# Optimization experiments

Measured on AMD Instinct MI355X. Metric: run time of the kernel, lower is better.

## Reference

```python
import jax, jax.numpy as jnp
import numpy as np

N = 150000   # nodes
E = 600000   # edges
F_IN = 32    # node features
H = 128      # hidden_channels == MLP_neurons
G = 2048     # graphs in batch


def setup_inputs() -> dict:
    key = jax.random.key(0)
    ks = iter(jax.random.split(key, 40))
    inp = {}
    inp['x'] = jax.random.normal(next(ks), (N, F_IN), dtype=jnp.float32)
    inp['edge_index'] = jax.random.randint(next(ks), (2, E), 0, N)
    inp['batch'] = jnp.sort(jax.random.randint(next(ks), (N,), 0, G))
    # GINConv MLPs: Linear(in,H) ReLU Linear(H,H) ReLU Linear(H,H)
    for i, f_in in enumerate([F_IN, H, H]):
        s1 = 1.0 / np.sqrt(f_in)
        s2 = 1.0 / np.sqrt(H)
        inp[f'c{i}_w1'] = jax.random.uniform(next(ks), (f_in, H), minval=-s1, maxval=s1)
        inp[f'c{i}_b1'] = jnp.zeros((H,), jnp.float32)
        inp[f'c{i}_w2'] = jax.random.uniform(next(ks), (H, H), minval=-s2, maxval=s2)
        inp[f'c{i}_b2'] = jnp.zeros((H,), jnp.float32)
        inp[f'c{i}_w3'] = jax.random.uniform(next(ks), (H, H), minval=-s2, maxval=s2)
        inp[f'c{i}_b3'] = jnp.zeros((H,), jnp.float32)
    s = 1.0 / np.sqrt(H)
    inp['fc0_w'] = jax.random.uniform(next(ks), (H, H), minval=-s, maxval=s)
    inp['fc0_b'] = jnp.zeros((H,), jnp.float32)
    inp['fc1_w'] = jax.random.uniform(next(ks), (H, H), minval=-s, maxval=s)
    inp['fc1_b'] = jnp.zeros((H,), jnp.float32)
    inp['out_w'] = jax.random.uniform(next(ks), (H, 2), minval=-s, maxval=s)
    inp['out_b'] = jnp.zeros((2,), jnp.float32)
    return inp


def _gin_layer(x, edge_index, w1, b1, w2, b2, w3, b3):
    # GINConv with eps=0: h = MLP(x + sum_{j in N(i)} x_j)
    agg = jax.ops.segment_sum(x[edge_index[0]], edge_index[1], num_segments=N)
    h = x + agg
    h = jax.nn.relu(h @ w1 + b1)
    h = jax.nn.relu(h @ w2 + b2)
    h = h @ w3 + b3
    return jax.nn.relu(h)  # outer .relu() in forward


def reference(x, edge_index, batch,
              c0_w1, c0_b1, c0_w2, c0_b2, c0_w3, c0_b3,
              c1_w1, c1_b1, c1_w2, c1_b2, c1_w3, c1_b3,
              c2_w1, c2_b1, c2_w2, c2_b2, c2_w3, c2_b3,
              fc0_w, fc0_b, fc1_w, fc1_b, out_w, out_b):
    h = _gin_layer(x, edge_index, c0_w1, c0_b1, c0_w2, c0_b2, c0_w3, c0_b3)
    h = _gin_layer(h, edge_index, c1_w1, c1_b1, c1_w2, c1_b2, c1_w3, c1_b3)
    h = _gin_layer(h, edge_index, c2_w1, c2_b1, c2_w2, c2_b2, c2_w3, c2_b3)
    # global_mean_pool over graph ids
    sums = jax.ops.segment_sum(h, batch, num_segments=G)            # [G,H]
    cnts = jax.ops.segment_sum(jnp.ones((N,), h.dtype), batch, num_segments=G)
    g = sums / jnp.maximum(cnts, 1.0)[:, None]
    # classifier head (dropout is identity at inference)
    g = jax.nn.relu(g @ fc0_w + fc0_b)
    g = jax.nn.relu(g @ fc1_w + fc1_b)
    return g @ out_w + out_b  # [G,2]
```

## Files before the change

### kernel.cpp

```cpp
#include <hip/hip_runtime.h>
#include <hip/hip_bf16.h>

#define NN 150000
#define EE 600000
#define F_IN 32
#define HD 128
#define GG 2048
#define CAP 28
#define NP 150016

typedef __attribute__((ext_vector_type(8))) short bf16x8;
typedef __attribute__((ext_vector_type(4))) float f32x4;

__device__ inline void split_bf16(float v, unsigned short& hi, unsigned short& lo) {
    __hip_bfloat16 h = __float2bfloat16(v);
    float hv = __bfloat162float(h);
    __hip_bfloat16 l = __float2bfloat16(v - hv);
    hi = *reinterpret_cast<unsigned short*>(&h);
    lo = *reinterpret_cast<unsigned short*>(&l);
}
__device__ inline unsigned short bf16_hi(float v) {
    __hip_bfloat16 h = __float2bfloat16(v);
    return *reinterpret_cast<unsigned short*>(&h);
}
__device__ inline unsigned short bf16_lo(float v) {
    __hip_bfloat16 h = __float2bfloat16(v);
    float hv = __bfloat162float(h);
    __hip_bfloat16 l = __float2bfloat16(v - hv);
    return *reinterpret_cast<unsigned short*>(&l);
}
__device__ inline float bf2f(unsigned short u) {
    union { unsigned int i; float f; } c;
    c.i = ((unsigned int)u) << 16;
    return c.f;
}

__global__ void init_zero(int* __restrict__ cnt_node, int* __restrict__ cntg,
                          float* __restrict__ pooled) {
    int i = blockIdx.x * blockDim.x + threadIdx.x;
    if (i < NN) cnt_node[i] = 0;
    if (i < GG) cntg[i] = 0;
    if (i < GG * HD) pooled[i] = 0.f;
}

__global__ void build_graph(const int* __restrict__ ei, const int* __restrict__ batch,
                            int* __restrict__ cnt_node, int* __restrict__ cntg,
                            int* __restrict__ bucket) {
    int e = blockIdx.x * blockDim.x + threadIdx.x;
    if (e < NN) atomicAdd(&cntg[batch[e]], 1);
    if (e >= EE) return;
    int src = ei[e];
    int dst = ei[EE + e];
    int slot = atomicAdd(&cnt_node[dst], 1);
    if (slot < CAP) bucket[dst * CAP + slot] = src;
}

struct PrepDesc { const float* src; unsigned short* dhi; unsigned short* dlo; int K; };
struct PrepArgs { PrepDesc d[9]; };

__global__ void prep_weights(PrepArgs pa) {
    PrepDesc de = pa.d[blockIdx.y];
    int total = de.K * HD;
    int KS = de.K >> 5;
    for (int idx = blockIdx.x * blockDim.x + threadIdx.x; idx < total;
         idx += gridDim.x * blockDim.x) {
        int k = idx / HD, h = idx - (idx / HD) * HD;
        unsigned short hi, lo;
        split_bf16(de.src[idx], hi, lo);
        int nt = h >> 4, m = h & 15;
        int ks = k >> 5, quad = (k >> 3) & 3, e = k & 7;
        int lane = quad * 16 + m;
        int pidx = ((nt * KS + ks) * 64 + lane) * 8 + e;
        de.dhi[pidx] = hi;
        de.dlo[pidx] = lo;
    }
}

template <int K_IN, bool BF16IN, bool POOL>
__launch_bounds__(256, 3)
__global__ void gin_layer(const void* __restrict__ hin_,
                          const int* __restrict__ cnt_node,
                          const int* __restrict__ bucket,
                          const unsigned short* __restrict__ w1h, const unsigned short* __restrict__ w1l,
                          const float* __restrict__ b1,
                          const unsigned short* __restrict__ w2h, const unsigned short* __restrict__ w2l,
                          const float* __restrict__ b2,
                          const unsigned short* __restrict__ w3h, const unsigned short* __restrict__ w3l,
                          const float* __restrict__ b3,
                          unsigned short* __restrict__ out,
                          const int* __restrict__ batch,
                          float* __restrict__ pooled) {
    constexpr int KS1 = K_IN / 32;
    constexpr int UN = BF16IN ? 4 : (KS1 == 1 ? 8 : 2);
    __shared__ unsigned short sh[4][32][HD + 8];

    const int wave = threadIdx.x >> 6;
    const int lane = threadIdx.x & 63;
    const int m = lane & 15;
    const int quad = lane >> 4;
    const int nodeBase = blockIdx.x * 128 + wave * 32;

    const float* hf = (const float*)hin_;
    const unsigned short* hb = (const unsigned short*)hin_;

    bf16x8 ah[2][KS1], al[2][KS1];
#pragma unroll
    for (int s = 0; s < 2; s++) {
        int node = nodeBase + s * 16 + m;
        node = node < NN ? node : NN - 1;
        float ag[KS1][8];
        if (BF16IN) {
            const unsigned short* rs = hb + (size_t)node * K_IN + quad * 8;
#pragma unroll
            for (int ks = 0; ks < KS1; ks++) {
                bf16x8 v = *(const bf16x8*)(rs + ks * 32);
#pragma unroll
                for (int e = 0; e < 8; e++) ag[ks][e] = bf2f((unsigned short)v[e]);
            }
        } else {
            const float* rs = hf + (size_t)node * K_IN + quad * 8;
#pragma unroll
            for (int ks = 0; ks < KS1; ks++) {
                float4 v0 = *(const float4*)(rs + ks * 32);
                float4 v1 = *(const float4*)(rs + ks * 32 + 4);
                ag[ks][0] = v0.x; ag[ks][1] = v0.y; ag[ks][2] = v0.z; ag[ks][3] = v0.w;
                ag[ks][4] = v1.x; ag[ks][5] = v1.y; ag[ks][6] = v1.z; ag[ks][7] = v1.w;
            }
        }
        int cnt = cnt_node[node];
        cnt = cnt < CAP ? cnt : CAP;
        const int* b = bucket + (size_t)node * CAP;
        int i = 0;
        if (BF16IN) {
            for (; i + UN <= cnt; i += UN) {
                bf16x8 v[UN][KS1];
#pragma unroll
                for (int j = 0; j < UN; j++) {
                    const unsigned short* r = hb + (size_t)b[i + j] * K_IN + quad * 8;
#pragma unroll
                    for (int ks = 0; ks < KS1; ks++)
                        v[j][ks] = *(const bf16x8*)(r + ks * 32);
                }
#pragma unroll
                for (int ks = 0; ks < KS1; ks++)
#pragma unroll
                    for (int e = 0; e < 8; e++) {
                        float t01 = bf2f((unsigned short)v[0][ks][e]) +
                                    bf2f((unsigned short)v[1][ks][e]);
                        float t23 = bf2f((unsigned short)v[2][ks][e]) +
                                    bf2f((unsigned short)v[3][ks][e]);
                        ag[ks][e] += t01 + t23;
                    }
            }
            for (; i < cnt; i++) {
                const unsigned short* r = hb + (size_t)b[i] * K_IN + quad * 8;
#pragma unroll
                for (int ks = 0; ks < KS1; ks++) {
                    bf16x8 v = *(const bf16x8*)(r + ks * 32);
#pragma unroll
                    for (int e = 0; e < 8; e++) ag[ks][e] += bf2f((unsigned short)v[e]);
                }
            }
        } else {
            for (; i + UN <= cnt; i += UN) {
                float4 v0[UN][KS1], v1[UN][KS1];
#pragma unroll
                for (int j = 0; j < UN; j++) {
                    const float* r = hf + (size_t)b[i + j] * K_IN + quad * 8;
#pragma unroll
                    for (int ks = 0; ks < KS1; ks++) {
                        v0[j][ks] = *(const float4*)(r + ks * 32);
                        v1[j][ks] = *(const float4*)(r + ks * 32 + 4);
                    }
                }
#pragma unroll
                for (int ks = 0; ks < KS1; ks++) {
#pragma unroll
                    for (int e = 0; e < 4; e++) {
                        float s01 = (&v0[0][ks].x)[e] + (&v0[1][ks].x)[e];
                        float s23 = (&v0[2][ks].x)[e] + (&v0[3][ks].x)[e];
                        if (UN == 8) {
                            s01 += (&v0[4][ks].x)[e] + (&v0[5][ks].x)[e];
                            s23 += (&v0[6][ks].x)[e] + (&v0[7][ks].x)[e];
                        }
                        ag[ks][e] += s01 + s23;
                    }
#pragma unroll
                    for (int e = 0; e < 4; e++) {
                        float s01 = (&v1[0][ks].x)[e] + (&v1[1][ks].x)[e];
                        float s23 = (&v1[2][ks].x)[e] + (&v1[3][ks].x)[e];
                        if (UN == 8) {
                            s01 += (&v1[4][ks].x)[e] + (&v1[5][ks].x)[e];
                            s23 += (&v1[6][ks].x)[e] + (&v1[7][ks].x)[e];
                        }
                        ag[ks][e + 4] += s01 + s23;
                    }
                }
            }
            for (; i < cnt; i++) {
                const float* r = hf + (size_t)b[i] * K_IN + quad * 8;
#pragma unroll
                for (int ks = 0; ks < KS1; ks++) {
                    float4 v0 = *(const float4*)(r + ks * 32);
                    float4 v1 = *(const float4*)(r + ks * 32 + 4);
                    ag[ks][0] += v0.x; ag[ks][1] += v0.y; ag[ks][2] += v0.z; ag[ks][3] += v0.w;
                    ag[ks][4] += v1.x; ag[ks][5] += v1.y; ag[ks][6] += v1.z; ag[ks][7] += v1.w;
                }
            }
        }
#pragma unroll
        for (int ks = 0; ks < KS1; ks++) {
            bf16x8 vh, vl;
#pragma unroll
            for (int e = 0; e < 8; e++) {
                unsigned short hi, lo;
                split_bf16(ag[ks][e], hi, lo);
                vh[e] = (short)hi;
                vl[e] = (short)lo;
            }
            ah[s][ks] = vh;
            al[s][ks] = vl;
        }
    }

    f32x4 acc[2][8];

#pragma unroll
    for (int nt = 0; nt < 8; nt++) {
        bf16x8 bh[KS1], bl[KS1];
#pragma unroll
        for (int ks = 0; ks < KS1; ks++) {
            bh[ks] = *(const bf16x8*)(w1h + ((nt * KS1 + ks) * 64 + lane) * 8);
            bl[ks] = *(const bf16x8*)(w1l + ((nt * KS1 + ks) * 64 + lane) * 8);
        }
        f32x4 c0 = {0.f, 0.f, 0.f, 0.f};
        f32x4 c1 = {0.f, 0.f, 0.f, 0.f};
#pragma unroll
        for (int ks = 0; ks < KS1; ks++) {
            c0 = __builtin_amdgcn_mfma_f32_16x16x32_bf16(ah[0][ks], bh[ks], c0, 0, 0, 0);
            c1 = __builtin_amdgcn_mfma_f32_16x16x32_bf16(ah[1][ks], bh[ks], c1, 0, 0, 0);
            c0 = __builtin_amdgcn_mfma_f32_16x16x32_bf16(al[0][ks], bh[ks], c0, 0, 0, 0);
            c1 = __builtin_amdgcn_mfma_f32_16x16x32_bf16(al[1][ks], bh[ks], c1, 0, 0, 0);
            c0 = __builtin_amdgcn_mfma_f32_16x16x32_bf16(ah[0][ks], bl[ks], c0, 0, 0, 0);
            c1 = __builtin_amdgcn_mfma_f32_16x16x32_bf16(ah[1][ks], bl[ks], c1, 0, 0, 0);
        }
        acc[0][nt] = c0;
        acc[1][nt] = c1;
    }

    bf16x8 a2h[2][4], a2l[2][4];
#pragma unroll
    for (int s = 0; s < 2; s++)
#pragma unroll
        for (int nt = 0; nt < 8; nt++) {
            float bj = b1[nt * 16 + m];
#pragma unroll
            for (int r = 0; r < 4; r++)
                sh[wave][s * 16 + quad * 4 + r][nt * 16 + m] =
                    bf16_hi(fmaxf(acc[s][nt][r] + bj, 0.f));
        }
#pragma unroll
    for (int s = 0; s < 2; s++)
#pragma unroll
        for (int ks = 0; ks < 4; ks++)
            a2h[s][ks] = *(const bf16x8*)&sh[wave][s * 16 + m][ks * 32 + quad * 8];
#pragma unroll
    for (int s = 0; s < 2; s++)
#pragma unroll
        for (int nt = 0; nt < 8; nt++) {
            float bj = b1[nt * 16 + m];
#pragma unroll
            for (int r = 0; r < 4; r++)
                sh[wave][s * 16 + quad * 4 + r][nt * 16 + m] =
                    bf16_lo(fmaxf(acc[s][nt][r] + bj, 0.f));
        }
#pragma unroll
    for (int s = 0; s < 2; s++)
#pragma unroll
        for (int ks = 0; ks < 4; ks++)
            a2l[s][ks] = *(const bf16x8*)&sh[wave][s * 16 + m][ks * 32 + quad * 8];

#pragma unroll
    for (int nt = 0; nt < 8; nt++) {
        bf16x8 bh[4], bl[4];
#pragma unroll
        for (int ks = 0; ks < 4; ks++) {
            bh[ks] = *(const bf16x8*)(w2h + ((nt * 4 + ks) * 64 + lane) * 8);
            bl[ks] = *(const bf16x8*)(w2l + ((nt * 4 + ks) * 64 + lane) * 8);
        }
        f32x4 c0 = {0.f, 0.f, 0.f, 0.f};
        f32x4 c1 = {0.f, 0.f, 0.f, 0.f};
#pragma unroll
        for (int ks = 0; ks < 4; ks++) {
            c0 = __builtin_amdgcn_mfma_f32_16x16x32_bf16(a2h[0][ks], bh[ks], c0, 0, 0, 0);
            c1 = __builtin_amdgcn_mfma_f32_16x16x32_bf16(a2h[1][ks], bh[ks], c1, 0, 0, 0);
            c0 = __builtin_amdgcn_mfma_f32_16x16x32_bf16(a2l[0][ks], bh[ks], c0, 0, 0, 0);
            c1 = __builtin_amdgcn_mfma_f32_16x16x32_bf16(a2l[1][ks], bh[ks], c1, 0, 0, 0);
            c0 = __builtin_amdgcn_mfma_f32_16x16x32_bf16(a2h[0][ks], bl[ks], c0, 0, 0, 0);
            c1 = __builtin_amdgcn_mfma_f32_16x16x32_bf16(a2h[1][ks], bl[ks], c1, 0, 0, 0);
        }
        acc[0][nt] = c0;
        acc[1][nt] = c1;
    }

#pragma unroll
    for (int s = 0; s < 2; s++)
#pragma unroll
        for (int nt = 0; nt < 8; nt++) {
            float bj = b2[nt * 16 + m];
#pragma unroll
            for (int r = 0; r < 4; r++)
                sh[wave][s * 16 + quad * 4 + r][nt * 16 + m] =
                    bf16_hi(fmaxf(acc[s][nt][r] + bj, 0.f));
        }
#pragma unroll
    for (int s = 0; s < 2; s++)
#pragma unroll
        for (int ks = 0; ks < 4; ks++)
            a2h[s][ks] = *(const bf16x8*)&sh[wave][s * 16 + m][ks * 32 + quad * 8];
#pragma unroll
    for (int s = 0; s < 2; s++)
#pragma unroll
        for (int nt = 0; nt < 8; nt++) {
            float bj = b2[nt * 16 + m];
#pragma unroll
            for (int r = 0; r < 4; r++)
                sh[wave][s * 16 + quad * 4 + r][nt * 16 + m] =
                    bf16_lo(fmaxf(acc[s][nt][r] + bj, 0.f));
        }
#pragma unroll
    for (int s = 0; s < 2; s++)
#pragma unroll
        for (int ks = 0; ks < 4; ks++)
            a2l[s][ks] = *(const bf16x8*)&sh[wave][s * 16 + m][ks * 32 + quad * 8];

#pragma unroll
    for (int nt = 0; nt < 8; nt++) {
        bf16x8 bh[4], bl[4];
#pragma unroll
        for (int ks = 0; ks < 4; ks++) {
            bh[ks] = *(const bf16x8*)(w3h + ((nt * 4 + ks) * 64 + lane) * 8);
            bl[ks] = *(const bf16x8*)(w3l + ((nt * 4 + ks) * 64 + lane) * 8);
        }
        f32x4 c0 = {0.f, 0.f, 0.f, 0.f};
        f32x4 c1 = {0.f, 0.f, 0.f, 0.f};
#pragma unroll
        for (int ks = 0; ks < 4; ks++) {
            c0 = __builtin_amdgcn_mfma_f32_16x16x32_bf16(a2h[0][ks], bh[ks], c0, 0, 0, 0);
            c1 = __builtin_amdgcn_mfma_f32_16x16x32_bf16(a2h[1][ks], bh[ks], c1, 0, 0, 0);
            c0 = __builtin_amdgcn_mfma_f32_16x16x32_bf16(a2l[0][ks], bh[ks], c0, 0, 0, 0);
            c1 = __builtin_amdgcn_mfma_f32_16x16x32_bf16(a2l[1][ks], bh[ks], c1, 0, 0, 0);
            c0 = __builtin_amdgcn_mfma_f32_16x16x32_bf16(a2h[0][ks], bl[ks], c0, 0, 0, 0);
            c1 = __builtin_amdgcn_mfma_f32_16x16x32_bf16(a2h[1][ks], bl[ks], c1, 0, 0, 0);
        }
        acc[0][nt] = c0;
        acc[1][nt] = c1;
    }

    if (POOL) {
        float* shf = (float*)&sh[wave][0][0];
#pragma unroll
        for (int h = 0; h < 2; h++) {
#pragma unroll
            for (int nt = 0; nt < 8; nt++) {
                float bj = b3[nt * 16 + m];
#pragma unroll
                for (int r = 0; r < 4; r++)
                    shf[(quad * 4 + r) * 132 + nt * 16 + m] =
                        fmaxf(acc[h][nt][r] + bj, 0.f);
            }
            int c0 = lane * 2;
            float run0 = 0.f, run1 = 0.f;
            int gp = -1;
            for (int rrow = 0; rrow < 16; rrow++) {
                int node = nodeBase + h * 16 + rrow;
                if (node >= NN) break;
                int g = batch[node];
                float2 xv = *(const float2*)&shf[rrow * 132 + c0];
                if (g != gp) {
                    if (gp >= 0) {
                        atomicAdd(&pooled[(size_t)gp * HD + c0 + 0], run0);
                        atomicAdd(&pooled[(size_t)gp * HD + c0 + 1], run1);
                    }
                    run0 = xv.x; run1 = xv.y; gp = g;
                } else {
                    run0 += xv.x; run1 += xv.y;
                }
            }
            if (gp >= 0) {
                atomicAdd(&pooled[(size_t)gp * HD + c0 + 0], run0);
                atomicAdd(&pooled[(size_t)gp * HD + c0 + 1], run1);
            }
        }
    } else {
#pragma unroll
        for (int s = 0; s < 2; s++)
#pragma unroll
            for (int nt = 0; nt < 8; nt++) {
                float bj = b3[nt * 16 + m];
#pragma unroll
                for (int r = 0; r < 4; r++)
                    sh[wave][s * 16 + quad * 4 + r][nt * 16 + m] =
                        bf16_hi(fmaxf(acc[s][nt][r] + bj, 0.f));
            }
#pragma unroll
        for (int io = 0; io < 8; io++) {
            int row32 = io * 4 + quad;
            int col = m * 8;
            int n2 = nodeBase + row32;
            bf16x8 v = *(const bf16x8*)&sh[wave][row32][col];
            if (n2 < NN) *(bf16x8*)&out[(size_t)n2 * HD + col] = v;
        }
    }
}

__launch_bounds__(128)
__global__ void head(const float* __restrict__ pooled, const int* __restrict__ cntg,
                     const float* __restrict__ fc0_w, const float* __restrict__ fc0_b,
                     const float* __restrict__ fc1_w, const float* __restrict__ fc1_b,
                     const float* __restrict__ out_w, const float* __restrict__ out_b,
                     float* __restrict__ out) {
    int g = blockIdx.x;
    int j = threadIdx.x;
    __shared__ float s0[HD];
    __shared__ float s1[HD];
    int c = cntg[g];
    float cf = (float)(c > 1 ? c : 1);
    s0[j] = pooled[(size_t)g * HD + j] / cf;
    __syncthreads();

    float acc = fc0_b[j];
    for (int k = 0; k < HD; k += 4) {
        float4 hv = *(const float4*)&s0[k];
        acc = fmaf(hv.x, fc0_w[(k + 0) * HD + j], acc);
        acc = fmaf(hv.y, fc0_w[(k + 1) * HD + j], acc);
        acc = fmaf(hv.z, fc0_w[(k + 2) * HD + j], acc);
        acc = fmaf(hv.w, fc0_w[(k + 3) * HD + j], acc);
    }
    s1[j] = fmaxf(acc, 0.0f);
    __syncthreads();

    acc = fc1_b[j];
    for (int k = 0; k < HD; k += 4) {
        float4 hv = *(const float4*)&s1[k];
        acc = fmaf(hv.x, fc1_w[(k + 0) * HD + j], acc);
        acc = fmaf(hv.y, fc1_w[(k + 1) * HD + j], acc);
        acc = fmaf(hv.z, fc1_w[(k + 2) * HD + j], acc);
        acc = fmaf(hv.w, fc1_w[(k + 3) * HD + j], acc);
    }
    float v = fmaxf(acc, 0.0f);

    float p0 = v * out_w[j * 2 + 0];
    float p1 = v * out_w[j * 2 + 1];
    __syncthreads();
    s0[j] = p0;
    s1[j] = p1;
    __syncthreads();
    for (int off = 64; off >= 1; off >>= 1) {
        if (j < off) {
            s0[j] += s0[j + off];
            s1[j] += s1[j + off];
        }
        __syncthreads();
    }
    if (j == 0) {
        out[(size_t)g * 2 + 0] = s0[0] + out_b[0];
        out[(size_t)g * 2 + 1] = s1[0] + out_b[1];
    }
}

extern "C" void kernel_launch(void* const* d_in, const int* in_sizes, int n_in,
                              void* d_out, int out_size, void* d_ws, size_t ws_size,
                              hipStream_t stream) {
    const float* x     = (const float*)d_in[0];
    const int*   ei    = (const int*)d_in[1];
    const int*   batch = (const int*)d_in[2];
    const float* cw[3][6];
    for (int i = 0; i < 3; i++)
        for (int k = 0; k < 6; k++) cw[i][k] = (const float*)d_in[3 + 6 * i + k];
    const float* fc0_w = (const float*)d_in[21];
    const float* fc0_b = (const float*)d_in[22];
    const float* fc1_w = (const float*)d_in[23];
    const float* fc1_b = (const float*)d_in[24];
    const float* out_w = (const float*)d_in[25];
    const float* out_b = (const float*)d_in[26];
    float* out = (float*)d_out;

    char* ws = (char*)d_ws;
    size_t off = 0;
    auto carve = [&](size_t bytes) {
        void* p = ws + off;
        off += (bytes + 255) & ~(size_t)255;
        return p;
    };
    int*   cnt_node = (int*)carve((size_t)NN * 4);
    int*   cntg     = (int*)carve((size_t)GG * 4);
    float* pooled   = (float*)carve((size_t)GG * HD * 4);
    int*   bucket   = (int*)carve((size_t)NN * CAP * 4);
    unsigned short* hA = (unsigned short*)carve((size_t)NP * HD * 2);
    unsigned short* hB = (unsigned short*)carve((size_t)NP * HD * 2);
    unsigned short* wHi[9];
    unsigned short* wLo[9];
    int wK[9] = {F_IN, HD, HD, HD, HD, HD, HD, HD, HD};
    for (int i = 0; i < 9; i++) {
        wHi[i] = (unsigned short*)carve((size_t)wK[i] * HD * 2);
        wLo[i] = (unsigned short*)carve((size_t)wK[i] * HD * 2);
    }
    (void)ws_size;

    init_zero<<<(GG * HD + 255) / 256, 256, 0, stream>>>(cnt_node, cntg, pooled);
    build_graph<<<(EE + 255) / 256, 256, 0, stream>>>(ei, batch, cnt_node, cntg, bucket);

    PrepArgs pa;
    for (int l = 0; l < 3; l++)
        for (int s = 0; s < 3; s++) {
            int i = l * 3 + s;
            pa.d[i].src = cw[l][2 * s];
            pa.d[i].dhi = wHi[i];
            pa.d[i].dlo = wLo[i];
            pa.d[i].K = wK[i];
        }
    prep_weights<<<dim3(16, 9), 256, 0, stream>>>(pa);

    const int blocks = NP / 128;

    gin_layer<F_IN, false, false><<<blocks, 256, 0, stream>>>(x, cnt_node, bucket,
        wHi[0], wLo[0], cw[0][1], wHi[1], wLo[1], cw[0][3], wHi[2], wLo[2], cw[0][5],
        hA, batch, pooled);
    gin_layer<HD, true, false><<<blocks, 256, 0, stream>>>(hA, cnt_node, bucket,
        wHi[3], wLo[3], cw[1][1], wHi[4], wLo[4], cw[1][3], wHi[5], wLo[5], cw[1][5],
        hB, batch, pooled);
    gin_layer<HD, true, true><<<blocks, 256, 0, stream>>>(hB, cnt_node, bucket,
        wHi[6], wLo[6], cw[2][1], wHi[7], wLo[7], cw[2][3], wHi[8], wLo[8], cw[2][5],
        nullptr, batch, pooled);

    head<<<GG, 128, 0, stream>>>(pooled, cntg, fc0_w, fc0_b, fc1_w, fc1_b, out_w, out_b, out);
}
```

Measured before the change: 547.2 us.

## Transpose neighbor bucket layout, replace graph-count atomics with binary search

```diff
diff --git a/kernel.cpp b/kernel.cpp
--- a/kernel.cpp
+++ b/kernel.cpp
@@ -35,24 +35,15 @@
     return c.f;
 }
 
-__global__ void init_zero(int* __restrict__ cnt_node, int* __restrict__ cntg,
-                          float* __restrict__ pooled) {
-    int i = blockIdx.x * blockDim.x + threadIdx.x;
-    if (i < NN) cnt_node[i] = 0;
-    if (i < GG) cntg[i] = 0;
-    if (i < GG * HD) pooled[i] = 0.f;
-}
-
-__global__ void build_graph(const int* __restrict__ ei, const int* __restrict__ batch,
-                            int* __restrict__ cnt_node, int* __restrict__ cntg,
+__global__ void build_graph(const int* __restrict__ ei,
+                            int* __restrict__ cnt_node,
                             int* __restrict__ bucket) {
     int e = blockIdx.x * blockDim.x + threadIdx.x;
-    if (e < NN) atomicAdd(&cntg[batch[e]], 1);
     if (e >= EE) return;
     int src = ei[e];
     int dst = ei[EE + e];
     int slot = atomicAdd(&cnt_node[dst], 1);
-    if (slot < CAP) bucket[dst * CAP + slot] = src;
+    if (slot < CAP) bucket[slot * NN + dst] = src;
 }
 
 struct PrepDesc { const float* src; unsigned short* dhi; unsigned short* dlo; int K; };
@@ -129,14 +120,14 @@
         }
         int cnt = cnt_node[node];
         cnt = cnt < CAP ? cnt : CAP;
-        const int* b = bucket + (size_t)node * CAP;
+        const int* b = bucket + node;
         int i = 0;
         if (BF16IN) {
             for (; i + UN <= cnt; i += UN) {
                 bf16x8 v[UN][KS1];
 #pragma unroll
                 for (int j = 0; j < UN; j++) {
-                    const unsigned short* r = hb + (size_t)b[i + j] * K_IN + quad * 8;
+                    const unsigned short* r = hb + (size_t)b[(i + j) * NN] * K_IN + quad * 8;
 #pragma unroll
                     for (int ks = 0; ks < KS1; ks++)
                         v[j][ks] = *(const bf16x8*)(r + ks * 32);
@@ -153,7 +144,7 @@
                     }
             }
             for (; i < cnt; i++) {
-                const unsigned short* r = hb + (size_t)b[i] * K_IN + quad * 8;
+                const unsigned short* r = hb + (size_t)b[i * NN] * K_IN + quad * 8;
 #pragma unroll
                 for (int ks = 0; ks < KS1; ks++) {
                     bf16x8 v = *(const bf16x8*)(r + ks * 32);
@@ -166,7 +157,7 @@
                 float4 v0[UN][KS1], v1[UN][KS1];
 #pragma unroll
                 for (int j = 0; j < UN; j++) {
-                    const float* r = hf + (size_t)b[i + j] * K_IN + quad * 8;
+                    const float* r = hf + (size_t)b[(i + j) * NN] * K_IN + quad * 8;
 #pragma unroll
                     for (int ks = 0; ks < KS1; ks++) {
                         v0[j][ks] = *(const float4*)(r + ks * 32);
@@ -198,7 +189,7 @@
                 }
             }
             for (; i < cnt; i++) {
-                const float* r = hf + (size_t)b[i] * K_IN + quad * 8;
+                const float* r = hf + (size_t)b[i * NN] * K_IN + quad * 8;
 #pragma unroll
                 for (int ks = 0; ks < KS1; ks++) {
                     float4 v0 = *(const float4*)(r + ks * 32);
@@ -414,8 +405,17 @@
     }
 }
 
+__device__ inline int lb_batch(const int* __restrict__ batch, int key) {
+    int lo = 0, hi = NN;
+    while (lo < hi) {
+        int mid = (lo + hi) >> 1;
+        if (batch[mid] < key) lo = mid + 1; else hi = mid;
+    }
+    return lo;
+}
+
 __launch_bounds__(128)
-__global__ void head(const float* __restrict__ pooled, const int* __restrict__ cntg,
+__global__ void head(const float* __restrict__ pooled, const int* __restrict__ batch,
                      const float* __restrict__ fc0_w, const float* __restrict__ fc0_b,
                      const float* __restrict__ fc1_w, const float* __restrict__ fc1_b,
                      const float* __restrict__ out_w, const float* __restrict__ out_b,
@@ -424,7 +424,7 @@
     int j = threadIdx.x;
     __shared__ float s0[HD];
     __shared__ float s1[HD];
-    int c = cntg[g];
+    int c = lb_batch(batch, g + 1) - lb_batch(batch, g);
     float cf = (float)(c > 1 ? c : 1);
     s0[j] = pooled[(size_t)g * HD + j] / cf;
     __syncthreads();
@@ -494,7 +494,6 @@
         return p;
     };
     int*   cnt_node = (int*)carve((size_t)NN * 4);
-    int*   cntg     = (int*)carve((size_t)GG * 4);
     float* pooled   = (float*)carve((size_t)GG * HD * 4);
     int*   bucket   = (int*)carve((size_t)NN * CAP * 4);
     unsigned short* hA = (unsigned short*)carve((size_t)NP * HD * 2);
@@ -508,8 +507,8 @@
     }
     (void)ws_size;
 
-    init_zero<<<(GG * HD + 255) / 256, 256, 0, stream>>>(cnt_node, cntg, pooled);
-    build_graph<<<(EE + 255) / 256, 256, 0, stream>>>(ei, batch, cnt_node, cntg, bucket);
+    hipMemsetAsync(cnt_node, 0, (size_t)((char*)bucket - (char*)cnt_node), stream);
+    build_graph<<<(EE + 255) / 256, 256, 0, stream>>>(ei, cnt_node, bucket);
 
     PrepArgs pa;
     for (int l = 0; l < 3; l++)
@@ -534,5 +533,5 @@
         wHi[6], wLo[6], cw[2][1], wHi[7], wLo[7], cw[2][3], wHi[8], wLo[8], cw[2][5],
         nullptr, batch, pooled);
 
-    head<<<GG, 128, 0, stream>>>(pooled, cntg, fc0_w, fc0_b, fc1_w, fc1_b, out_w, out_b, out);
-}
+    head<<<GG, 128, 0, stream>>>(pooled, batch, fc0_w, fc0_b, fc1_w, fc1_b, out_w, out_b, out);
+}
```

Result: faster. 520.5 us (-4.9%).
